# Optimization experiments

Hardware: AMD Instinct MI355X
Metric: run time of the kernel (lower is better)

## Reference

```python
import jax, jax.numpy as jnp
import numpy as np

V = 100000   # vocab size
H = 1280     # GRU hidden / pic_emb_size
E = 300      # word_emb_size
L = 32       # max_length


def setup_inputs() -> dict:
    key = jax.random.key(0)
    ks = jax.random.split(key, 7)
    s = 0.02  # weight init scale
    return {
        "hidden0": jax.random.normal(ks[0], (H,), jnp.float32),
        "start_emb": jax.random.normal(ks[1], (E,), jnp.float32),
        "W_ih": jax.random.normal(ks[2], (3 * H, E), jnp.float32) * s,
        "W_hh": jax.random.normal(ks[3], (3 * H, H), jnp.float32) * s,
        "b_ih": jnp.zeros((3 * H,), jnp.float32),
        "b_hh": jnp.zeros((3 * H,), jnp.float32),
        "W_cls": jax.random.normal(ks[4], (V, H), jnp.float32) * s,
        "b_cls": jnp.zeros((V,), jnp.float32),
        "vocab_vectors": jax.random.normal(ks[5], (V, E), jnp.float32),
        "max_length": L,
    }


def reference(hidden0, start_emb, W_ih, W_hh, b_ih, b_hh, W_cls, b_cls,
              vocab_vectors, max_length):
    """Autoregressive GRU decode: GRU step -> 1280x100k classifier GEMV ->
    argmax -> embedding gather, for max_length steps (batch=1).
    EOS (token 0) emulated with a `done` mask instead of a Python break.
    Returns (tokens [L] int32, hiddens [L, H] float32)."""

    def step(carry, _):
        h, emb, done = carry
        # PyTorch GRU gate layout: [reset | update | new]
        gi = W_ih @ emb + b_ih               # [3H]
        gh = W_hh @ h + b_hh                 # [3H]
        r = jax.nn.sigmoid(gi[:H] + gh[:H])
        z = jax.nn.sigmoid(gi[H:2 * H] + gh[H:2 * H])
        n = jnp.tanh(gi[2 * H:] + r * gh[2 * H:])
        h_new = jnp.where(done, h, (1.0 - z) * n + z * h)
        logits = W_cls @ h_new + b_cls       # [V] classifier GEMV
        pred = jnp.argmax(logits).astype(jnp.int32)
        token = jnp.where(done, 0, pred)
        done_new = done | (pred == 0)
        emb_new = jnp.where(done_new, emb, vocab_vectors[pred])  # gather next word emb
        return (h_new, emb_new, done_new), (token, h_new)

    init = (hidden0, start_emb, jnp.array(False))
    _, (tokens, hiddens) = jax.lax.scan(step, init, None, length=max_length)
    return tokens, hiddens
```

## Files before the change

### kernel.cpp

```cpp
#include <hip/hip_runtime.h>
#include <math.h>
#include <limits.h>

#define V 100000
#define H 1280
#define E 300
#define L 32
#define NBLK 1563

#define WS_H0     0
#define WS_H1     1280
#define WS_EMB    2560
#define WS_SUMA   2880
#define WS_SUMB   3008
#define WS_DONE0  3136
#define WS_DONE1  3137
#define WS_LOGITS 3140
#define WS_SROW   (WS_LOGITS + V)
#define WS_PLO    (WS_SROW + V)
#define WS_PHI    (WS_PLO + NBLK)
#define WS_Q_BYTEOFF 825088
#define WS_BYTES_NEEDED (WS_Q_BYTEOFF + (size_t)V * H)
#define CAND_CAP 256
#define PBLK_CAP 128

#define FB_GI     4000
#define FB_GH     (FB_GI + 3840)
#define FB_NPART  6250
#define FB_PVAL   12000
#define FB_PIDX   (FB_PVAL + FB_NPART)

__global__ __launch_bounds__(256)
void init_state(const float* __restrict__ hidden0, const float* __restrict__ start_emb,
                float* __restrict__ ws) {
    int i = blockIdx.x * blockDim.x + threadIdx.x;
    if (i < H) { ws[WS_H0 + i] = hidden0[i]; ws[WS_H1 + i] = hidden0[i]; }
    if (i < E) ws[WS_EMB + i] = start_emb[i];
    if (i < 8) { ws[WS_SUMA + i * 16] = 0.f; ws[WS_SUMB + i * 16] = 0.f; }
    if (i == 0) { ((int*)ws)[WS_DONE0] = 0; ((int*)ws)[WS_DONE1] = 0; }
}

__global__ __launch_bounds__(256)
void convert_int8(const float* __restrict__ W, uint* __restrict__ q_out,
                  float* __restrict__ ws) {
    const int wave = threadIdx.x >> 6;
    const int lane = threadIdx.x & 63;
    const int row = blockIdx.x * 4 + wave;
    const float4* __restrict__ wr = (const float4*)(W + (size_t)row * H);

    float4 v[5];
    float mx = 0.f;
    #pragma unroll
    for (int k = 0; k < 5; ++k) {
        v[k] = wr[lane + 64*k];
        mx = fmaxf(mx, fmaxf(fmaxf(fabsf(v[k].x), fabsf(v[k].y)),
                             fmaxf(fabsf(v[k].z), fabsf(v[k].w))));
    }
    #pragma unroll
    for (int off = 32; off; off >>= 1) mx = fmaxf(mx, __shfl_xor(mx, off));

    float inv = (mx > 0.f) ? 127.0f / mx : 0.f;
    float s   = (mx > 0.f) ? mx / 127.0f : 0.f;

    uint* __restrict__ qrow = q_out + (size_t)row * (H/4);
    #pragma unroll
    for (int k = 0; k < 5; ++k) {
        int q0 = max(-127, min(127, __float2int_rn(v[k].x * inv)));
        int q1 = max(-127, min(127, __float2int_rn(v[k].y * inv)));
        int q2 = max(-127, min(127, __float2int_rn(v[k].z * inv)));
        int q3 = max(-127, min(127, __float2int_rn(v[k].w * inv)));
        qrow[lane + 64*k] = (uint)(q0 & 0xff) | ((uint)(q1 & 0xff) << 8) |
                            ((uint)(q2 & 0xff) << 16) | ((uint)(q3 & 0xff) << 24);
    }
    if (lane == 0) ws[WS_SROW + row] = s;
}

__global__ __launch_bounds__(256)
void fin_gru(const float* __restrict__ W_ih, const float* __restrict__ W_hh,
             const float* __restrict__ b_ih, const float* __restrict__ b_hh,
             const float* __restrict__ W_cls, const float* __restrict__ b_cls,
             const float* __restrict__ vocab, const float* __restrict__ start_emb,
             float* __restrict__ ws, float* __restrict__ out,
             float* __restrict__ hid_out, int k) {
    __shared__ float red[256];
    __shared__ int   npass, cnt;
    __shared__ int   pblk[PBLK_CAP];
    __shared__ int   cidx[CAND_CAP];
    __shared__ float cval[CAND_CAP];
    __shared__ int   s_pred, s_done;
    __shared__ __align__(16) float emb_s[304];

    const int tid  = threadIdx.x;
    const int wave = tid >> 6;
    const int lane = tid & 63;

    const float* hin  = ws + ((k & 1) ^ 1) * H;
    float*       hout = ws + (k & 1) * H;

    if (k == 0) {
        for (int i = tid; i < E; i += 256) emb_s[i] = start_emb[i];
        if (tid == 0) s_done = 0;
        __syncthreads();
    } else {
        const int sslot = ((k - 1) & 1) ? WS_SUMB : WS_SUMA;
        float sumabs = 0.f;
        #pragma unroll
        for (int i = 0; i < 8; ++i) sumabs += ws[sslot + i * 16];

        float m = -INFINITY;
        for (int b = tid; b < NBLK; b += 256) m = fmaxf(m, ws[WS_PLO + b]);
        red[tid] = m;
        __syncthreads();
        for (int s = 128; s; s >>= 1) {
            if (tid < s) red[tid] = fmaxf(red[tid], red[tid + s]);
            __syncthreads();
        }
        m = red[0];
        if (tid == 0) { npass = 0; cnt = 0; }
        __syncthreads();

        for (int b = tid; b < NBLK; b += 256) {
            if (ws[WS_PHI + b] >= m) {
                int p = atomicAdd(&npass, 1);
                if (p < PBLK_CAP) pblk[p] = b;
            }
        }
        __syncthreads();
        const int np = min(npass, PBLK_CAP);

        for (int j = tid; j < np * 64; j += 256) {
            int row = pblk[j >> 6] * 64 + (j & 63);
            if (row < V) {
                float s = ws[WS_SROW + row];
                float e = 0.501f * s * sumabs + 0.002f;
                if (ws[WS_LOGITS + row] + e >= m) {
                    int p = atomicAdd(&cnt, 1);
                    if (p < CAND_CAP) cidx[p] = row;
                }
            }
        }
        __syncthreads();
        const int nc = min(cnt, CAND_CAP);

        const float4* h4r = (const float4*)hin;
        for (int c = wave; c < nc; c += 4) {
            int row = cidx[c];
            const float4* wr = (const float4*)(W_cls + (size_t)row * H);
            float s = 0.f;
            #pragma unroll
            for (int kk = 0; kk < 5; ++kk) {
                float4 wv = wr[lane + 64*kk], hv = h4r[lane + 64*kk];
                s += wv.x*hv.x + wv.y*hv.y + wv.z*hv.z + wv.w*hv.w;
            }
            #pragma unroll
            for (int off = 32; off; off >>= 1) s += __shfl_down(s, off);
            if (lane == 0) cval[c] = s + b_cls[row];
        }
        __syncthreads();

        if (tid == 0) {
            float bv = -INFINITY; int bi = INT_MAX;
            for (int c = 0; c < nc; ++c) {
                float v = cval[c]; int i = cidx[c];
                if (v > bv || (v == bv && i < bi)) { bv = v; bi = i; }
            }
            int pred = bi;
            int done_in = (k >= 2) ? ((const int*)ws)[(k & 1) ? WS_DONE1 : WS_DONE0] : 0;
            if (blockIdx.x == 0) out[k - 1] = (float)(done_in ? 0 : pred);
            int dn = done_in | (pred == 0);
            ((int*)ws)[((k - 1) & 1) ? WS_DONE1 : WS_DONE0] = dn;
            s_pred = pred; s_done = dn;
        }
        __syncthreads();
        const int pr = s_pred;
        for (int i = tid; i < E; i += 256) emb_s[i] = vocab[(size_t)pr * E + i];
        __syncthreads();
    }

    const int u = blockIdx.x * 4 + wave;
    const float4* emb4 = (const float4*)emb_s;
    const float4* h4 = (const float4*)hin;
    float4 hv[5];
    #pragma unroll
    for (int kk = 0; kk < 5; ++kk) hv[kk] = h4[lane + 64*kk];

    float si0 = 0.f, si1 = 0.f, si2 = 0.f, sh0 = 0.f, sh1 = 0.f, sh2 = 0.f;
    {
        const float4* w0 = (const float4*)(W_ih + (size_t)u * E);
        const float4* w1 = (const float4*)(W_ih + (size_t)(H + u) * E);
        const float4* w2 = (const float4*)(W_ih + (size_t)(2*H + u) * E);
        for (int i = lane; i < 75; i += 64) {
            float4 e = emb4[i];
            float4 a = w0[i]; si0 += a.x*e.x + a.y*e.y + a.z*e.z + a.w*e.w;
            float4 b = w1[i]; si1 += b.x*e.x + b.y*e.y + b.z*e.z + b.w*e.w;
            float4 c = w2[i]; si2 += c.x*e.x + c.y*e.y + c.z*e.z + c.w*e.w;
        }
        const float4* v0 = (const float4*)(W_hh + (size_t)u * H);
        const float4* v1 = (const float4*)(W_hh + (size_t)(H + u) * H);
        const float4* v2 = (const float4*)(W_hh + (size_t)(2*H + u) * H);
        #pragma unroll
        for (int kk = 0; kk < 5; ++kk) {
            float4 a = v0[lane + 64*kk];
            sh0 += a.x*hv[kk].x + a.y*hv[kk].y + a.z*hv[kk].z + a.w*hv[kk].w;
            float4 b = v1[lane + 64*kk];
            sh1 += b.x*hv[kk].x + b.y*hv[kk].y + b.z*hv[kk].z + b.w*hv[kk].w;
            float4 c = v2[lane + 64*kk];
            sh2 += c.x*hv[kk].x + c.y*hv[kk].y + c.z*hv[kk].z + c.w*hv[kk].w;
        }
    }
    #pragma unroll
    for (int off = 32; off; off >>= 1) {
        si0 += __shfl_down(si0, off); si1 += __shfl_down(si1, off);
        si2 += __shfl_down(si2, off);
        sh0 += __shfl_down(sh0, off); sh1 += __shfl_down(sh1, off);
        sh2 += __shfl_down(sh2, off);
    }
    if (lane == 0) {
        float r = 1.f / (1.f + expf(-(si0 + b_ih[u]       + sh0 + b_hh[u])));
        float z = 1.f / (1.f + expf(-(si1 + b_ih[H + u]   + sh1 + b_hh[H + u])));
        float n = tanhf(si2 + b_ih[2*H + u] + r * (sh2 + b_hh[2*H + u]));
        float hold = hin[u];
        float hnew = s_done ? hold : (1.f - z) * n + z * hold;
        hout[u] = hnew;
        hid_out[u] = hnew;
        const int aslot = (k & 1) ? WS_SUMB : WS_SUMA;
        atomicAdd(ws + aslot + (u & 7) * 16, fabsf(hnew));
    }
}

__global__ __launch_bounds__(256)
void cls_int8(const uint* __restrict__ Q, const float* __restrict__ b_cls,
              float* __restrict__ ws, const float* __restrict__ h, int k) {
    if (blockIdx.x == 0 && threadIdx.x < 8)
        ws[(((k + 1) & 1) ? WS_SUMB : WS_SUMA) + threadIdx.x * 16] = 0.f;

    const int wave = threadIdx.x >> 6;
    const int lane = threadIdx.x & 63;
    const int row0 = blockIdx.x * 64 + wave * 16;
    const float4* __restrict__ h4 = (const float4*)h;

    float4 hv[5];
    #pragma unroll
    for (int kk = 0; kk < 5; ++kk) hv[kk] = h4[lane + 64*kk];

    const int sslot = (k & 1) ? WS_SUMB : WS_SUMA;
    float sumabs = 0.f;
    #pragma unroll
    for (int i = 0; i < 8; ++i) sumabs += ws[sslot + i * 16];

    float wlo = -INFINITY, whi = -INFINITY;
    for (int rr = 0; rr < 16; ++rr) {
        const int row = row0 + rr;
        if (row >= V) break;
        const uint* __restrict__ qr = Q + (size_t)row * (H/4);
        float acc = 0.f;
        #pragma unroll
        for (int kk = 0; kk < 5; ++kk) {
            uint u = qr[lane + 64*kk];
            float f0 = (float)((int)(u << 24) >> 24);
            float f1 = (float)((int)(u << 16) >> 24);
            float f2 = (float)((int)(u <<  8) >> 24);
            float f3 = (float)((int) u        >> 24);
            acc += f0*hv[kk].x + f1*hv[kk].y + f2*hv[kk].z + f3*hv[kk].w;
        }
        #pragma unroll
        for (int off = 32; off; off >>= 1) acc += __shfl_down(acc, off);
        if (lane == 0) {
            float s = ws[WS_SROW + row];
            float q = s * acc + b_cls[row];
            ws[WS_LOGITS + row] = q;
            float e = 0.501f * s * sumabs + 0.002f;
            wlo = fmaxf(wlo, q - e);
            whi = fmaxf(whi, q + e);
        }
    }
    __shared__ float slo[4], shi[4];
    if (lane == 0) { slo[wave] = wlo; shi[wave] = whi; }
    __syncthreads();
    if (threadIdx.x == 0) {
        ws[WS_PLO + blockIdx.x] = fmaxf(fmaxf(slo[0], slo[1]), fmaxf(slo[2], slo[3]));
        ws[WS_PHI + blockIdx.x] = fmaxf(fmaxf(shi[0], shi[1]), fmaxf(shi[2], shi[3]));
    }
}

__global__ __launch_bounds__(256)
void finalize_tail(float* __restrict__ ws, const float* __restrict__ W_cls,
                   const float* __restrict__ b_cls, float* __restrict__ out) {
    __shared__ float red[256];
    __shared__ int   npass, cnt;
    __shared__ int   pblk[PBLK_CAP];
    __shared__ int   cidx[CAND_CAP];
    __shared__ float cval[CAND_CAP];
    const int tid = threadIdx.x;
    const int wave = tid >> 6, lane = tid & 63;

    float sumabs = 0.f;
    #pragma unroll
    for (int i = 0; i < 8; ++i) sumabs += ws[WS_SUMB + i * 16];

    float m = -INFINITY;
    for (int b = tid; b < NBLK; b += 256) m = fmaxf(m, ws[WS_PLO + b]);
    red[tid] = m;
    __syncthreads();
    for (int s = 128; s; s >>= 1) {
        if (tid < s) red[tid] = fmaxf(red[tid], red[tid + s]);
        __syncthreads();
    }
    m = red[0];
    if (tid == 0) { npass = 0; cnt = 0; }
    __syncthreads();

    for (int b = tid; b < NBLK; b += 256) {
        if (ws[WS_PHI + b] >= m) {
            int p = atomicAdd(&npass, 1);
            if (p < PBLK_CAP) pblk[p] = b;
        }
    }
    __syncthreads();
    const int np = min(npass, PBLK_CAP);

    for (int j = tid; j < np * 64; j += 256) {
        int row = pblk[j >> 6] * 64 + (j & 63);
        if (row < V) {
            float s = ws[WS_SROW + row];
            float e = 0.501f * s * sumabs + 0.002f;
            if (ws[WS_LOGITS + row] + e >= m) {
                int p = atomicAdd(&cnt, 1);
                if (p < CAND_CAP) cidx[p] = row;
            }
        }
    }
    __syncthreads();
    const int nc = min(cnt, CAND_CAP);

    const float4* h4 = (const float4*)(ws + WS_H1);
    for (int c = wave; c < nc; c += 4) {
        int row = cidx[c];
        const float4* wr = (const float4*)(W_cls + (size_t)row * H);
        float s = 0.f;
        #pragma unroll
        for (int kk = 0; kk < 5; ++kk) {
            float4 wv = wr[lane + 64*kk], hv = h4[lane + 64*kk];
            s += wv.x*hv.x + wv.y*hv.y + wv.z*hv.z + wv.w*hv.w;
        }
        #pragma unroll
        for (int off = 32; off; off >>= 1) s += __shfl_down(s, off);
        if (lane == 0) cval[c] = s + b_cls[row];
    }
    __syncthreads();

    if (tid == 0) {
        float bv = -INFINITY; int bi = INT_MAX;
        for (int c = 0; c < nc; ++c) {
            float v = cval[c]; int i = cidx[c];
            if (v > bv || (v == bv && i < bi)) { bv = v; bi = i; }
        }
        int done_in = ((const int*)ws)[WS_DONE0];
        out[L - 1] = (float)(done_in ? 0 : bi);
    }
}

__global__ __launch_bounds__(256)
void fb_gru_matvec(const float* __restrict__ W_ih, const float* __restrict__ W_hh,
                   const float* __restrict__ b_ih, const float* __restrict__ b_hh,
                   float* __restrict__ ws) {
    const int wave = threadIdx.x >> 6;
    const int lane = threadIdx.x & 63;
    const int row = blockIdx.x * 4 + wave;
    const float4* __restrict__ emb4 = (const float4*)(ws + WS_EMB);
    const float4* __restrict__ h4   = (const float4*)(ws + WS_H0);
    const float4* __restrict__ wi = (const float4*)(W_ih + (size_t)row * E);
    float s1 = 0.f;
    for (int i = lane; i < 75; i += 64) {
        float4 w = wi[i], e = emb4[i];
        s1 += w.x*e.x + w.y*e.y + w.z*e.z + w.w*e.w;
    }
    const float4* __restrict__ wh = (const float4*)(W_hh + (size_t)row * H);
    float s2 = 0.f;
    #pragma unroll
    for (int k = 0; k < 5; ++k) {
        float4 w = wh[lane + 64*k], hv = h4[lane + 64*k];
        s2 += w.x*hv.x + w.y*hv.y + w.z*hv.z + w.w*hv.w;
    }
    #pragma unroll
    for (int off = 32; off; off >>= 1) {
        s1 += __shfl_down(s1, off);
        s2 += __shfl_down(s2, off);
    }
    if (lane == 0) {
        ws[FB_GI + row] = s1 + b_ih[row];
        ws[FB_GH + row] = s2 + b_hh[row];
    }
}

__global__ __launch_bounds__(256)
void fb_gru_combine(float* __restrict__ ws, float* __restrict__ hid_out) {
    int j = blockIdx.x * 256 + threadIdx.x;
    if (j >= H) return;
    int done = ((const int*)ws)[WS_DONE0];
    float gir = ws[FB_GI + j], giz = ws[FB_GI + H + j], gin = ws[FB_GI + 2*H + j];
    float ghr = ws[FB_GH + j], ghz = ws[FB_GH + H + j], ghn = ws[FB_GH + 2*H + j];
    float r = 1.f / (1.f + expf(-(gir + ghr)));
    float z = 1.f / (1.f + expf(-(giz + ghz)));
    float n = tanhf(gin + r * ghn);
    float hold = ws[WS_H0 + j];
    float hnew = done ? hold : (1.f - z) * n + z * hold;
    ws[WS_H0 + j] = hnew;
    hid_out[j] = hnew;
}

__global__ __launch_bounds__(256)
void fb_logits_argmax(const float* __restrict__ W_cls, const float* __restrict__ b_cls,
                      float* __restrict__ ws) {
    const int wave = threadIdx.x >> 6;
    const int lane = threadIdx.x & 63;
    const int row0 = blockIdx.x * 16 + wave * 4;
    const float4* __restrict__ h4 = (const float4*)(ws + WS_H0);
    float best = -INFINITY;
    int bidx = INT_MAX;
    for (int rr = 0; rr < 4; ++rr) {
        const int row = row0 + rr;
        const float4* __restrict__ wr = (const float4*)(W_cls + (size_t)row * H);
        float s = 0.f;
        #pragma unroll
        for (int k = 0; k < 5; ++k) {
            float4 w = wr[lane + 64*k], hv = h4[lane + 64*k];
            s += w.x*hv.x + w.y*hv.y + w.z*hv.z + w.w*hv.w;
        }
        #pragma unroll
        for (int off = 32; off; off >>= 1) s += __shfl_down(s, off);
        if (lane == 0) {
            float logit = s + b_cls[row];
            if (logit > best) { best = logit; bidx = row; }
        }
    }
    __shared__ float sval[4];
    __shared__ int   sidx[4];
    if (lane == 0) { sval[wave] = best; sidx[wave] = bidx; }
    __syncthreads();
    if (threadIdx.x == 0) {
        float bv = sval[0]; int bi = sidx[0];
        #pragma unroll
        for (int w = 1; w < 4; ++w)
            if (sval[w] > bv || (sval[w] == bv && sidx[w] < bi)) { bv = sval[w]; bi = sidx[w]; }
        ws[FB_PVAL + blockIdx.x] = bv;
        ((int*)ws)[FB_PIDX + blockIdx.x] = bi;
    }
}

__global__ __launch_bounds__(1024)
void fb_argmax_update(float* __restrict__ ws, const float* __restrict__ vocab,
                      float* __restrict__ tok_out, int t) {
    __shared__ float sval[1024];
    __shared__ int   sidx[1024];
    const int tid = threadIdx.x;
    float best = -INFINITY;
    int bidx = INT_MAX;
    for (int i = tid; i < FB_NPART; i += 1024) {
        float v = ws[FB_PVAL + i];
        int  id = ((const int*)ws)[FB_PIDX + i];
        if (v > best || (v == best && id < bidx)) { best = v; bidx = id; }
    }
    sval[tid] = best; sidx[tid] = bidx;
    __syncthreads();
    #pragma unroll
    for (int s = 512; s; s >>= 1) {
        if (tid < s) {
            if (sval[tid+s] > sval[tid] ||
                (sval[tid+s] == sval[tid] && sidx[tid+s] < sidx[tid])) {
                sval[tid] = sval[tid+s]; sidx[tid] = sidx[tid+s];
            }
        }
        __syncthreads();
    }
    __shared__ int s_pred, s_donenew;
    if (tid == 0) {
        int pred = sidx[0];
        int done = ((const int*)ws)[WS_DONE0];
        tok_out[t] = (float)(done ? 0 : pred);
        int done_new = done | (pred == 0);
        ((int*)ws)[WS_DONE0] = done_new;
        s_pred = pred; s_donenew = done_new;
    }
    __syncthreads();
    if (!s_donenew && tid < E)
        ws[WS_EMB + tid] = vocab[(size_t)s_pred * E + tid];
}

extern "C" void kernel_launch(void* const* d_in, const int* in_sizes, int n_in,
                              void* d_out, int out_size, void* d_ws, size_t ws_size,
                              hipStream_t stream) {
    const float* hidden0   = (const float*)d_in[0];
    const float* start_emb = (const float*)d_in[1];
    const float* W_ih      = (const float*)d_in[2];
    const float* W_hh      = (const float*)d_in[3];
    const float* b_ih      = (const float*)d_in[4];
    const float* b_hh      = (const float*)d_in[5];
    const float* W_cls     = (const float*)d_in[6];
    const float* b_cls     = (const float*)d_in[7];
    const float* vocab     = (const float*)d_in[8];
    float* out = (float*)d_out;
    float* ws  = (float*)d_ws;

    hipLaunchKernelGGL(init_state, dim3(5), dim3(256), 0, stream, hidden0, start_emb, ws);

    if (ws_size >= WS_BYTES_NEEDED) {
        uint* Q = (uint*)((char*)d_ws + WS_Q_BYTEOFF);
        hipLaunchKernelGGL(convert_int8, dim3(V/4), dim3(256), 0, stream, W_cls, Q, ws);
        for (int k = 0; k < L; ++k) {
            const float* hk = ws + (k & 1) * H;
            hipLaunchKernelGGL(fin_gru, dim3(H/4), dim3(256), 0, stream,
                               W_ih, W_hh, b_ih, b_hh, W_cls, b_cls, vocab,
                               start_emb, ws, out, out + L + (size_t)k * H, k);
            hipLaunchKernelGGL(cls_int8, dim3(NBLK), dim3(256), 0, stream,
                               Q, b_cls, ws, hk, k);
        }
        hipLaunchKernelGGL(finalize_tail, dim3(1), dim3(256), 0, stream,
                           ws, W_cls, b_cls, out);
    } else {
        for (int t = 0; t < L; ++t) {
            hipLaunchKernelGGL(fb_gru_matvec, dim3(960), dim3(256), 0, stream,
                               W_ih, W_hh, b_ih, b_hh, ws);
            hipLaunchKernelGGL(fb_gru_combine, dim3(5), dim3(256), 0, stream,
                               ws, out + L + (size_t)t * H);
            hipLaunchKernelGGL(fb_logits_argmax, dim3(FB_NPART), dim3(256), 0, stream,
                               W_cls, b_cls, ws);
            hipLaunchKernelGGL(fb_argmax_update, dim3(1), dim3(1024), 0, stream,
                               ws, vocab, out, t);
        }
    }
}
```

Measured before the change: 1.670 ms.

## Split GRU gate rows across waves with one hidden unit per block

The fused finalize+GRU kernel now launches H blocks instead of H/4. Each block handles a single hidden unit, with three waves each computing one gate row's dot products, and the partial results are combined through shared memory. This spreads the W_hh/W_ih streaming over more blocks to raise memory parallelism. The cost is that the per-block prologue (argmax finalization over candidates and the embedding gather) is repeated four times as often, and one wave per block sits idle.

```diff
diff --git a/kernel.cpp b/kernel.cpp
--- a/kernel.cpp
+++ b/kernel.cpp
@@ -88,6 +88,7 @@
     __shared__ int   cidx[CAND_CAP];
     __shared__ float cval[CAND_CAP];
     __shared__ int   s_pred, s_done;
+    __shared__ float gi_s[3], gh_s[3];
     __shared__ __align__(16) float emb_s[304];
 
     const int tid  = threadIdx.x;
@@ -177,54 +178,46 @@
         __syncthreads();
     }
 
-    const int u = blockIdx.x * 4 + wave;
-    const float4* emb4 = (const float4*)emb_s;
-    const float4* h4 = (const float4*)hin;
-    float4 hv[5];
-    #pragma unroll
-    for (int kk = 0; kk < 5; ++kk) hv[kk] = h4[lane + 64*kk];
-
-    float si0 = 0.f, si1 = 0.f, si2 = 0.f, sh0 = 0.f, sh1 = 0.f, sh2 = 0.f;
-    {
-        const float4* w0 = (const float4*)(W_ih + (size_t)u * E);
-        const float4* w1 = (const float4*)(W_ih + (size_t)(H + u) * E);
-        const float4* w2 = (const float4*)(W_ih + (size_t)(2*H + u) * E);
+    const int j = blockIdx.x;
+    if (wave < 3) {
+        const int row = wave * H + j;
+        const float4* emb4 = (const float4*)emb_s;
+        const float4* h4   = (const float4*)hin;
+
+        const float4* wi = (const float4*)(W_ih + (size_t)row * E);
+        float si = 0.f;
         for (int i = lane; i < 75; i += 64) {
-            float4 e = emb4[i];
-            float4 a = w0[i]; si0 += a.x*e.x + a.y*e.y + a.z*e.z + a.w*e.w;
-            float4 b = w1[i]; si1 += b.x*e.x + b.y*e.y + b.z*e.z + b.w*e.w;
-            float4 c = w2[i]; si2 += c.x*e.x + c.y*e.y + c.z*e.z + c.w*e.w;
-        }
-        const float4* v0 = (const float4*)(W_hh + (size_t)u * H);
-        const float4* v1 = (const float4*)(W_hh + (size_t)(H + u) * H);
-        const float4* v2 = (const float4*)(W_hh + (size_t)(2*H + u) * H);
+            float4 w = wi[i], e = emb4[i];
+            si += w.x*e.x + w.y*e.y + w.z*e.z + w.w*e.w;
+        }
+        const float4* wh = (const float4*)(W_hh + (size_t)row * H);
+        float sh = 0.f;
         #pragma unroll
         for (int kk = 0; kk < 5; ++kk) {
-            float4 a = v0[lane + 64*kk];
-            sh0 += a.x*hv[kk].x + a.y*hv[kk].y + a.z*hv[kk].z + a.w*hv[kk].w;
-            float4 b = v1[lane + 64*kk];
-            sh1 += b.x*hv[kk].x + b.y*hv[kk].y + b.z*hv[kk].z + b.w*hv[kk].w;
-            float4 c = v2[lane + 64*kk];
-            sh2 += c.x*hv[kk].x + c.y*hv[kk].y + c.z*hv[kk].z + c.w*hv[kk].w;
-        }
-    }
-    #pragma unroll
-    for (int off = 32; off; off >>= 1) {
-        si0 += __shfl_down(si0, off); si1 += __shfl_down(si1, off);
-        si2 += __shfl_down(si2, off);
-        sh0 += __shfl_down(sh0, off); sh1 += __shfl_down(sh1, off);
-        sh2 += __shfl_down(sh2, off);
-    }
-    if (lane == 0) {
-        float r = 1.f / (1.f + expf(-(si0 + b_ih[u]       + sh0 + b_hh[u])));
-        float z = 1.f / (1.f + expf(-(si1 + b_ih[H + u]   + sh1 + b_hh[H + u])));
-        float n = tanhf(si2 + b_ih[2*H + u] + r * (sh2 + b_hh[2*H + u]));
-        float hold = hin[u];
+            float4 w = wh[lane + 64*kk], hv = h4[lane + 64*kk];
+            sh += w.x*hv.x + w.y*hv.y + w.z*hv.z + w.w*hv.w;
+        }
+        #pragma unroll
+        for (int off = 32; off; off >>= 1) {
+            si += __shfl_down(si, off);
+            sh += __shfl_down(sh, off);
+        }
+        if (lane == 0) {
+            gi_s[wave] = si + b_ih[row];
+            gh_s[wave] = sh + b_hh[row];
+        }
+    }
+    __syncthreads();
+    if (tid == 0) {
+        float r = 1.f / (1.f + expf(-(gi_s[0] + gh_s[0])));
+        float z = 1.f / (1.f + expf(-(gi_s[1] + gh_s[1])));
+        float n = tanhf(gi_s[2] + r * gh_s[2]);
+        float hold = hin[j];
         float hnew = s_done ? hold : (1.f - z) * n + z * hold;
-        hout[u] = hnew;
-        hid_out[u] = hnew;
+        hout[j] = hnew;
+        hid_out[j] = hnew;
         const int aslot = (k & 1) ? WS_SUMB : WS_SUMA;
-        atomicAdd(ws + aslot + (u & 7) * 16, fabsf(hnew));
+        atomicAdd(ws + aslot + (j & 7) * 16, fabsf(hnew));
     }
 }
 
@@ -509,7 +502,7 @@
         hipLaunchKernelGGL(convert_int8, dim3(V/4), dim3(256), 0, stream, W_cls, Q, ws);
         for (int k = 0; k < L; ++k) {
             const float* hk = ws + (k & 1) * H;
-            hipLaunchKernelGGL(fin_gru, dim3(H/4), dim3(256), 0, stream,
+            hipLaunchKernelGGL(fin_gru, dim3(H), dim3(256), 0, stream,
                                W_ih, W_hh, b_ih, b_hh, W_cls, b_cls, vocab,
                                start_emb, ws, out, out + L + (size_t)k * H, k);
             hipLaunchKernelGGL(cls_int8, dim3(NBLK), dim3(256), 0, stream,
```

New measurement: 1.717 ms. 1.03x slower.
